# Performance work log

Hardware: AMD Instinct MI355X
Metric: run time of the kernel (lower is better)

The kernel has to match this reference:

```python
import jax, jax.numpy as jnp
import numpy as np

P = 2  # pooling_size

def setup_inputs() -> dict:
    key = jax.random.key(0)
    k1, k2, k3 = jax.random.split(key, 3)
    B, n, D = 16, 4096, 1024
    x = jax.random.normal(k1, (B, n, D), dtype=jnp.float32)
    W1 = jax.random.normal(k2, (D, D), dtype=jnp.float32) * (1.0 / np.sqrt(D))
    b1 = jnp.zeros((D,), dtype=jnp.float32)
    W2 = jax.random.normal(k3, (D, 1), dtype=jnp.float32) * (1.0 / np.sqrt(D))
    b2 = jnp.zeros((1,), dtype=jnp.float32)
    return {"x": x, "W1": W1, "b1": b1, "W2": W2, "b2": b2}

def reference(x, W1, b1, W2, b2):
    # x: [B, n, D] with n a perfect square; pool 2x2 windows via attention.
    B, n, D = x.shape
    s = int(n ** 0.5)
    g = s // P  # grid of regions per side
    # [B, g, P, g, P, D] -> [B, g, g, P, P, D] -> [B, R, P*P, D]
    # region order matches the original double loop (row-major over i, j).
    xg = (x.reshape(B, g, P, g, P, D)
            .transpose(0, 1, 3, 2, 4, 5)
            .reshape(B, g * g, P * P, D))
    # MLP scores (dropout is identity in eval mode)
    h = jax.nn.relu(jnp.einsum('brkd,de->brke', xg, W1) + b1)
    logits = jnp.einsum('brkd,d->brk', h, W2[:, 0]) + b2[0]
    alpha = jax.nn.softmax(logits, axis=-1)  # softmax over the P*P window
    # weighted sum over window -> [B, R, D]
    return jnp.einsum('brk,brkd->brd', alpha, xg)
```

## Files before the change

### kernel.cpp

```cpp
#include <hip/hip_runtime.h>
#include <hip/hip_bf16.h>

typedef float f32x4 __attribute__((ext_vector_type(4)));
typedef __bf16 bf16x8 __attribute__((ext_vector_type(8)));
typedef unsigned short ushort_t;
typedef ushort_t u16x8 __attribute__((ext_vector_type(8)));

#define GLDS16(gp, lp)                                                        \
  __builtin_amdgcn_global_load_lds(                                           \
      (__attribute__((address_space(1))) void*)(gp),                          \
      (__attribute__((address_space(3))) void*)(lp), 16, 0, 0)

__device__ __forceinline__ ushort_t f2bf(float f) {
  unsigned u = __float_as_uint(f);
  unsigned r = u + 0x7fffu + ((u >> 16) & 1u);
  return (ushort_t)(r >> 16);
}

__device__ __forceinline__ int swz(int row) {
  return (row & 3) ^ ((row >> 2) & 3);
}

__global__ __launch_bounds__(256) void prep_w1(const float* __restrict__ w1,
                                               ushort_t* __restrict__ w1t) {
  __shared__ ushort_t tile[64][80];
  const int k0 = blockIdx.x * 64;
  const int n0 = blockIdx.y * 64;
  const int tid = threadIdx.x;
#pragma unroll
  for (int it = 0; it < 16; ++it) {
    int idx = it * 256 + tid;
    int k = idx >> 6, n = idx & 63;
    tile[n][k] = f2bf(w1[(size_t)(k0 + k) * 1024 + n0 + n]);
  }
  __syncthreads();
#pragma unroll
  for (int it = 0; it < 2; ++it) {
    int idx = it * 256 + tid;
    int n = idx >> 3, kk = (idx & 7) * 8;
    bf16x8 v = *(const bf16x8*)&tile[n][kk];
    *(bf16x8*)&w1t[(size_t)(n0 + n) * 1024 + k0 + kk] = v;
  }
}

__global__ __launch_bounds__(256) void prep_x(const float* __restrict__ x,
                                              ushort_t* __restrict__ xbf) {
  size_t i = ((size_t)blockIdx.x * 256 + threadIdx.x) * 8;
  float4 a = *(const float4*)(x + i);
  float4 b = *(const float4*)(x + i + 4);
  u16x8 o;
  o[0] = f2bf(a.x); o[1] = f2bf(a.y); o[2] = f2bf(a.z); o[3] = f2bf(a.w);
  o[4] = f2bf(b.x); o[5] = f2bf(b.y); o[6] = f2bf(b.z); o[7] = f2bf(b.w);
  *(u16x8*)(xbf + i) = o;
}

#define FOLD_EPILOGUE(ACC, NH)                                                \
  {                                                                           \
    float bv[4], wv[4];                                                       \
    _Pragma("unroll") for (int ni = 0; ni < 4; ++ni) {                        \
      int col = nt * 256 + (NH)*128 + wn + ni * 16 + lc;                      \
      bv[ni] = b1[col];                                                       \
      wv[ni] = w2[col];                                                       \
    }                                                                         \
    _Pragma("unroll") for (int mi = 0; mi < 4; ++mi)                          \
        _Pragma("unroll") for (int r = 0; r < 4; ++r) {                       \
      float s = 0.f;                                                          \
      _Pragma("unroll") for (int ni = 0; ni < 4; ++ni) {                      \
        float h = ACC[mi][ni][r] + bv[ni];                                    \
        h = h > 0.f ? h : 0.f;                                                \
        s += h * wv[ni];                                                      \
      }                                                                       \
      racc[mi][r] += s;                                                       \
    }                                                                         \
  }

template <bool A_BF16>
__global__ __launch_bounds__(256, 2) void gemm_fused(
    const void* __restrict__ aglob, const ushort_t* __restrict__ w1t,
    const float* __restrict__ b1, const float* __restrict__ w2,
    const float* __restrict__ x, float* __restrict__ out) {
  __shared__ ushort_t As[2][128 * 32];
  __shared__ ushort_t Bs0[2][128 * 32];
  __shared__ ushort_t Bs1[2][128 * 32];
  __shared__ float lbuf[128];
  __shared__ float abuf[128];

  const int tid = threadIdx.x;
  const int wave = tid >> 6, lane = tid & 63;
  const int quad = lane >> 4, lc = lane & 15;
  const int m0 = blockIdx.x * 128;
  const int wm = (wave & 1) * 64, wn = (wave >> 1) * 64;

  const int g0 = tid, g1 = 256 + tid;
  const int r0 = g0 >> 2, c0 = (g0 & 3) ^ swz(g0 >> 2);
  const int r1 = g1 >> 2, c1 = (g1 & 3) ^ swz(g1 >> 2);
  const ushort_t* abf0 = nullptr; const ushort_t* abf1 = nullptr;
  const float* af0 = nullptr; const float* af1 = nullptr;
  if constexpr (A_BF16) {
    abf0 = (const ushort_t*)aglob + (size_t)(m0 + r0) * 1024 + c0 * 8;
    abf1 = (const ushort_t*)aglob + (size_t)(m0 + r1) * 1024 + c1 * 8;
  } else {
    af0 = (const float*)aglob + (size_t)(m0 + r0) * 1024 + c0 * 8;
    af1 = (const float*)aglob + (size_t)(m0 + r1) * 1024 + c1 * 8;
  }
  const ushort_t* b00 = w1t + (size_t)r0 * 1024 + c0 * 8;
  const ushort_t* b01 = w1t + (size_t)r1 * 1024 + c1 * 8;
  const ushort_t* b10 = w1t + (size_t)(128 + r0) * 1024 + c0 * 8;
  const ushort_t* b11 = w1t + (size_t)(128 + r1) * 1024 + c1 * 8;

  int aoff[4], boff[4];
#pragma unroll
  for (int mi = 0; mi < 4; ++mi) {
    int r = wm + mi * 16 + lc;
    aoff[mi] = r * 32 + (quad ^ swz(r)) * 8;
  }
#pragma unroll
  for (int ni = 0; ni < 4; ++ni) {
    int r = wn + ni * 16 + lc;
    boff[ni] = r * 32 + (quad ^ swz(r)) * 8;
  }

  auto stage = [&](int buf, int nt_, int kt_) {
    const size_t cb = (size_t)nt_ * (256 * 1024);
    const int k0 = kt_ * 32;
    GLDS16(b00 + cb + k0, &Bs0[buf][g0 * 8]);
    GLDS16(b01 + cb + k0, &Bs0[buf][g1 * 8]);
    GLDS16(b10 + cb + k0, &Bs1[buf][g0 * 8]);
    GLDS16(b11 + cb + k0, &Bs1[buf][g1 * 8]);
    if constexpr (A_BF16) {
      GLDS16(abf0 + k0, &As[buf][g0 * 8]);
      GLDS16(abf1 + k0, &As[buf][g1 * 8]);
    } else {
      const int k0f = kt_ * 32;
      float4 v0 = *(const float4*)(af0 + k0f);
      float4 v1 = *(const float4*)(af0 + k0f + 4);
      float4 v2 = *(const float4*)(af1 + k0f);
      float4 v3 = *(const float4*)(af1 + k0f + 4);
      u16x8 o0, o1;
      o0[0] = f2bf(v0.x); o0[1] = f2bf(v0.y); o0[2] = f2bf(v0.z); o0[3] = f2bf(v0.w);
      o0[4] = f2bf(v1.x); o0[5] = f2bf(v1.y); o0[6] = f2bf(v1.z); o0[7] = f2bf(v1.w);
      o1[0] = f2bf(v2.x); o1[1] = f2bf(v2.y); o1[2] = f2bf(v2.z); o1[3] = f2bf(v2.w);
      o1[4] = f2bf(v3.x); o1[5] = f2bf(v3.y); o1[6] = f2bf(v3.z); o1[7] = f2bf(v3.w);
      *(u16x8*)&As[buf][g0 * 8] = o0;
      *(u16x8*)&As[buf][g1 * 8] = o1;
    }
  };

  float racc[4][4] = {};

  stage(0, 0, 0);
  __syncthreads();

  for (int nt = 0; nt < 4; ++nt) {
    f32x4 acc0[4][4] = {};
    f32x4 acc1[4][4] = {};
#pragma unroll 2
    for (int kt = 0; kt < 32; ++kt) {
      const int cur = kt & 1;
      if (!(nt == 3 && kt == 31)) {
        int nk = kt + 1, nn = nt;
        if (nk == 32) { nk = 0; nn = nt + 1; }
        stage(cur ^ 1, nn, nk);
      }

      bf16x8 afr[4], bfr0[4], bfr1[4];
#pragma unroll
      for (int mi = 0; mi < 4; ++mi) afr[mi] = *(const bf16x8*)&As[cur][aoff[mi]];
#pragma unroll
      for (int ni = 0; ni < 4; ++ni) {
        bfr0[ni] = *(const bf16x8*)&Bs0[cur][boff[ni]];
        bfr1[ni] = *(const bf16x8*)&Bs1[cur][boff[ni]];
      }
#pragma unroll
      for (int mi = 0; mi < 4; ++mi)
#pragma unroll
        for (int ni = 0; ni < 4; ++ni) {
          acc0[mi][ni] = __builtin_amdgcn_mfma_f32_16x16x32_bf16(
              afr[mi], bfr0[ni], acc0[mi][ni], 0, 0, 0);
          acc1[mi][ni] = __builtin_amdgcn_mfma_f32_16x16x32_bf16(
              afr[mi], bfr1[ni], acc1[mi][ni], 0, 0, 0);
        }
      __syncthreads();
    }
    FOLD_EPILOGUE(acc0, 0)
    FOLD_EPILOGUE(acc1, 1)
  }

#pragma unroll
  for (int mi = 0; mi < 4; ++mi)
#pragma unroll
    for (int r = 0; r < 4; ++r)
#pragma unroll
      for (int off = 1; off < 16; off <<= 1)
        racc[mi][r] += __shfl_xor(racc[mi][r], off, 64);
  __syncthreads();
  if (tid < 128) lbuf[tid] = 0.f;
  __syncthreads();
  if (lc == 0) {
#pragma unroll
    for (int mi = 0; mi < 4; ++mi)
#pragma unroll
      for (int r = 0; r < 4; ++r)
        atomicAdd(&lbuf[wm + mi * 16 + quad * 4 + r], racc[mi][r]);
  }
  __syncthreads();

  if (tid < 32) {
    const int j = tid;
    float l0 = lbuf[2 * j], l1 = lbuf[2 * j + 1];
    float l2 = lbuf[64 + 2 * j], l3 = lbuf[65 + 2 * j];
    float mx = fmaxf(fmaxf(l0, l1), fmaxf(l2, l3));
    float e0 = __expf(l0 - mx), e1 = __expf(l1 - mx);
    float e2 = __expf(l2 - mx), e3 = __expf(l3 - mx);
    float inv = 1.0f / (e0 + e1 + e2 + e3);
    abuf[j * 4 + 0] = e0 * inv;
    abuf[j * 4 + 1] = e1 * inv;
    abuf[j * 4 + 2] = e2 * inv;
    abuf[j * 4 + 3] = e3 * inv;
  }
  __syncthreads();

  const int b = blockIdx.x >> 5, ii = blockIdx.x & 31;
  const float* xs = x + (size_t)m0 * 1024;
  float* orow = out + ((size_t)(b * 1024 + ii * 32)) * 1024;
  for (int j = 0; j < 32; ++j) {
    float a0 = abuf[j * 4 + 0], a1 = abuf[j * 4 + 1];
    float a2 = abuf[j * 4 + 2], a3 = abuf[j * 4 + 3];
    const float4* p0 = (const float4*)(xs + (size_t)(2 * j) * 1024);
    const float4* p1 = (const float4*)(xs + (size_t)(2 * j + 1) * 1024);
    const float4* p2 = (const float4*)(xs + (size_t)(64 + 2 * j) * 1024);
    const float4* p3 = (const float4*)(xs + (size_t)(65 + 2 * j) * 1024);
    float4 v0 = p0[tid], v1 = p1[tid], v2 = p2[tid], v3 = p3[tid];
    float4 o;
    o.x = a0 * v0.x + a1 * v1.x + a2 * v2.x + a3 * v3.x;
    o.y = a0 * v0.y + a1 * v1.y + a2 * v2.y + a3 * v3.y;
    o.z = a0 * v0.z + a1 * v1.z + a2 * v2.z + a3 * v3.z;
    o.w = a0 * v0.w + a1 * v1.w + a2 * v2.w + a3 * v3.w;
    ((float4*)(orow + (size_t)j * 1024))[tid] = o;
  }
}

extern "C" void kernel_launch(void* const* d_in, const int* in_sizes, int n_in,
                              void* d_out, int out_size, void* d_ws,
                              size_t ws_size, hipStream_t stream) {
  const float* x  = (const float*)d_in[0];
  const float* W1 = (const float*)d_in[1];
  const float* b1 = (const float*)d_in[2];
  const float* W2 = (const float*)d_in[3];
  float* out = (float*)d_out;

  const size_t XBF_BYTES = 134217728ull;
  const size_t W1T_BYTES = 2097152ull;

  if (ws_size >= XBF_BYTES + W1T_BYTES) {
    ushort_t* xbf = (ushort_t*)d_ws;
    ushort_t* w1t = (ushort_t*)((char*)d_ws + XBF_BYTES);
    prep_x<<<32768, 256, 0, stream>>>(x, xbf);
    prep_w1<<<dim3(16, 16), 256, 0, stream>>>(W1, w1t);
    gemm_fused<true><<<512, 256, 0, stream>>>(xbf, w1t, b1, W2, x, out);
  } else {
    ushort_t* w1t = (ushort_t*)d_ws;
    prep_w1<<<dim3(16, 16), 256, 0, stream>>>(W1, w1t);
    gemm_fused<false><<<512, 256, 0, stream>>>(x, w1t, b1, W2, x, out);
  }
}
```

Baseline: 583.2 us.

## Split fused GEMM block across eight waves with halved per-wave N tile

Doubles the block from 256 to 512 threads. Each wave now computes one 64x64 accumulator tile instead of two, and the two B sub-buffers are merged into one 256-row LDS tile. Global-to-LDS staging and the final weighted-sum loop are spread over the larger thread count. The aim is lower per-wave register pressure and more resident waves to hide memory and MFMA latency. In exchange, each A fragment is now read from LDS by twice as many waves, and the 512,4 launch bound may force spills if 128 VGPRs is not enough.

```diff
diff --git a/kernel.cpp b/kernel.cpp
--- a/kernel.cpp
+++ b/kernel.cpp
@@ -54,11 +54,11 @@
   *(u16x8*)(xbf + i) = o;
 }
 
-#define FOLD_EPILOGUE(ACC, NH)                                                \
+#define FOLD_EPILOGUE(ACC)                                                    \
   {                                                                           \
     float bv[4], wv[4];                                                       \
     _Pragma("unroll") for (int ni = 0; ni < 4; ++ni) {                        \
-      int col = nt * 256 + (NH)*128 + wn + ni * 16 + lc;                      \
+      int col = nt * 256 + wn + ni * 16 + lc;                                 \
       bv[ni] = b1[col];                                                       \
       wv[ni] = w2[col];                                                       \
     }                                                                         \
@@ -75,13 +75,12 @@
   }
 
 template <bool A_BF16>
-__global__ __launch_bounds__(256, 2) void gemm_fused(
+__global__ __launch_bounds__(512, 4) void gemm_fused(
     const void* __restrict__ aglob, const ushort_t* __restrict__ w1t,
     const float* __restrict__ b1, const float* __restrict__ w2,
     const float* __restrict__ x, float* __restrict__ out) {
   __shared__ ushort_t As[2][128 * 32];
-  __shared__ ushort_t Bs0[2][128 * 32];
-  __shared__ ushort_t Bs1[2][128 * 32];
+  __shared__ ushort_t Bs[2][256 * 32];
   __shared__ float lbuf[128];
   __shared__ float abuf[128];
 
@@ -91,22 +90,19 @@
   const int m0 = blockIdx.x * 128;
   const int wm = (wave & 1) * 64, wn = (wave >> 1) * 64;
 
-  const int g0 = tid, g1 = 256 + tid;
-  const int r0 = g0 >> 2, c0 = (g0 & 3) ^ swz(g0 >> 2);
-  const int r1 = g1 >> 2, c1 = (g1 & 3) ^ swz(g1 >> 2);
-  const ushort_t* abf0 = nullptr; const ushort_t* abf1 = nullptr;
-  const float* af0 = nullptr; const float* af1 = nullptr;
+  const int rA = tid >> 2, cA = (tid & 3) ^ swz(tid >> 2);
+  const int rB0 = tid >> 2, cB0 = (tid & 3) ^ swz(rB0);
+  const int rB1 = 128 + (tid >> 2), cB1 = (tid & 3) ^ swz(rB1);
+
+  const ushort_t* abf = nullptr;
+  const float* af = nullptr;
   if constexpr (A_BF16) {
-    abf0 = (const ushort_t*)aglob + (size_t)(m0 + r0) * 1024 + c0 * 8;
-    abf1 = (const ushort_t*)aglob + (size_t)(m0 + r1) * 1024 + c1 * 8;
+    abf = (const ushort_t*)aglob + (size_t)(m0 + rA) * 1024 + cA * 8;
   } else {
-    af0 = (const float*)aglob + (size_t)(m0 + r0) * 1024 + c0 * 8;
-    af1 = (const float*)aglob + (size_t)(m0 + r1) * 1024 + c1 * 8;
-  }
-  const ushort_t* b00 = w1t + (size_t)r0 * 1024 + c0 * 8;
-  const ushort_t* b01 = w1t + (size_t)r1 * 1024 + c1 * 8;
-  const ushort_t* b10 = w1t + (size_t)(128 + r0) * 1024 + c0 * 8;
-  const ushort_t* b11 = w1t + (size_t)(128 + r1) * 1024 + c1 * 8;
+    af = (const float*)aglob + (size_t)(m0 + rA) * 1024 + cA * 8;
+  }
+  const ushort_t* bp0 = w1t + (size_t)rB0 * 1024 + cB0 * 8;
+  const ushort_t* bp1 = w1t + (size_t)rB1 * 1024 + cB1 * 8;
 
   int aoff[4], boff[4];
 #pragma unroll
@@ -123,26 +119,17 @@
   auto stage = [&](int buf, int nt_, int kt_) {
     const size_t cb = (size_t)nt_ * (256 * 1024);
     const int k0 = kt_ * 32;
-    GLDS16(b00 + cb + k0, &Bs0[buf][g0 * 8]);
-    GLDS16(b01 + cb + k0, &Bs0[buf][g1 * 8]);
-    GLDS16(b10 + cb + k0, &Bs1[buf][g0 * 8]);
-    GLDS16(b11 + cb + k0, &Bs1[buf][g1 * 8]);
+    GLDS16(bp0 + cb + k0, &Bs[buf][tid * 8]);
+    GLDS16(bp1 + cb + k0, &Bs[buf][(512 + tid) * 8]);
     if constexpr (A_BF16) {
-      GLDS16(abf0 + k0, &As[buf][g0 * 8]);
-      GLDS16(abf1 + k0, &As[buf][g1 * 8]);
+      GLDS16(abf + k0, &As[buf][tid * 8]);
     } else {
-      const int k0f = kt_ * 32;
-      float4 v0 = *(const float4*)(af0 + k0f);
-      float4 v1 = *(const float4*)(af0 + k0f + 4);
-      float4 v2 = *(const float4*)(af1 + k0f);
-      float4 v3 = *(const float4*)(af1 + k0f + 4);
-      u16x8 o0, o1;
+      float4 v0 = *(const float4*)(af + k0);
+      float4 v1 = *(const float4*)(af + k0 + 4);
+      u16x8 o0;
       o0[0] = f2bf(v0.x); o0[1] = f2bf(v0.y); o0[2] = f2bf(v0.z); o0[3] = f2bf(v0.w);
       o0[4] = f2bf(v1.x); o0[5] = f2bf(v1.y); o0[6] = f2bf(v1.z); o0[7] = f2bf(v1.w);
-      o1[0] = f2bf(v2.x); o1[1] = f2bf(v2.y); o1[2] = f2bf(v2.z); o1[3] = f2bf(v2.w);
-      o1[4] = f2bf(v3.x); o1[5] = f2bf(v3.y); o1[6] = f2bf(v3.z); o1[7] = f2bf(v3.w);
-      *(u16x8*)&As[buf][g0 * 8] = o0;
-      *(u16x8*)&As[buf][g1 * 8] = o1;
+      *(u16x8*)&As[buf][tid * 8] = o0;
     }
   };
 
@@ -152,8 +139,7 @@
   __syncthreads();
 
   for (int nt = 0; nt < 4; ++nt) {
-    f32x4 acc0[4][4] = {};
-    f32x4 acc1[4][4] = {};
+    f32x4 acc[4][4] = {};
 #pragma unroll 2
     for (int kt = 0; kt < 32; ++kt) {
       const int cur = kt & 1;
@@ -163,27 +149,20 @@
         stage(cur ^ 1, nn, nk);
       }
 
-      bf16x8 afr[4], bfr0[4], bfr1[4];
+      bf16x8 afr[4], bfr[4];
 #pragma unroll
       for (int mi = 0; mi < 4; ++mi) afr[mi] = *(const bf16x8*)&As[cur][aoff[mi]];
 #pragma unroll
-      for (int ni = 0; ni < 4; ++ni) {
-        bfr0[ni] = *(const bf16x8*)&Bs0[cur][boff[ni]];
-        bfr1[ni] = *(const bf16x8*)&Bs1[cur][boff[ni]];
-      }
+      for (int ni = 0; ni < 4; ++ni) bfr[ni] = *(const bf16x8*)&Bs[cur][boff[ni]];
 #pragma unroll
       for (int mi = 0; mi < 4; ++mi)
 #pragma unroll
-        for (int ni = 0; ni < 4; ++ni) {
-          acc0[mi][ni] = __builtin_amdgcn_mfma_f32_16x16x32_bf16(
-              afr[mi], bfr0[ni], acc0[mi][ni], 0, 0, 0);
-          acc1[mi][ni] = __builtin_amdgcn_mfma_f32_16x16x32_bf16(
-              afr[mi], bfr1[ni], acc1[mi][ni], 0, 0, 0);
-        }
+        for (int ni = 0; ni < 4; ++ni)
+          acc[mi][ni] = __builtin_amdgcn_mfma_f32_16x16x32_bf16(
+              afr[mi], bfr[ni], acc[mi][ni], 0, 0, 0);
       __syncthreads();
     }
-    FOLD_EPILOGUE(acc0, 0)
-    FOLD_EPILOGUE(acc1, 1)
+    FOLD_EPILOGUE(acc)
   }
 
 #pragma unroll
@@ -221,22 +200,24 @@
   __syncthreads();
 
   const int b = blockIdx.x >> 5, ii = blockIdx.x & 31;
+  const int jj = tid >> 8, t = tid & 255;
   const float* xs = x + (size_t)m0 * 1024;
   float* orow = out + ((size_t)(b * 1024 + ii * 32)) * 1024;
-  for (int j = 0; j < 32; ++j) {
+  for (int j0 = 0; j0 < 32; j0 += 2) {
+    int j = j0 + jj;
     float a0 = abuf[j * 4 + 0], a1 = abuf[j * 4 + 1];
     float a2 = abuf[j * 4 + 2], a3 = abuf[j * 4 + 3];
     const float4* p0 = (const float4*)(xs + (size_t)(2 * j) * 1024);
     const float4* p1 = (const float4*)(xs + (size_t)(2 * j + 1) * 1024);
     const float4* p2 = (const float4*)(xs + (size_t)(64 + 2 * j) * 1024);
     const float4* p3 = (const float4*)(xs + (size_t)(65 + 2 * j) * 1024);
-    float4 v0 = p0[tid], v1 = p1[tid], v2 = p2[tid], v3 = p3[tid];
+    float4 v0 = p0[t], v1 = p1[t], v2 = p2[t], v3 = p3[t];
     float4 o;
     o.x = a0 * v0.x + a1 * v1.x + a2 * v2.x + a3 * v3.x;
     o.y = a0 * v0.y + a1 * v1.y + a2 * v2.y + a3 * v3.y;
     o.z = a0 * v0.z + a1 * v1.z + a2 * v2.z + a3 * v3.z;
     o.w = a0 * v0.w + a1 * v1.w + a2 * v2.w + a3 * v3.w;
-    ((float4*)(orow + (size_t)j * 1024))[tid] = o;
+    ((float4*)(orow + (size_t)j * 1024))[t] = o;
   }
 }
 
@@ -257,10 +238,10 @@
     ushort_t* w1t = (ushort_t*)((char*)d_ws + XBF_BYTES);
     prep_x<<<32768, 256, 0, stream>>>(x, xbf);
     prep_w1<<<dim3(16, 16), 256, 0, stream>>>(W1, w1t);
-    gemm_fused<true><<<512, 256, 0, stream>>>(xbf, w1t, b1, W2, x, out);
+    gemm_fused<true><<<512, 512, 0, stream>>>(xbf, w1t, b1, W2, x, out);
   } else {
     ushort_t* w1t = (ushort_t*)d_ws;
     prep_w1<<<dim3(16, 16), 256, 0, stream>>>(W1, w1t);
-    gemm_fused<false><<<512, 256, 0, stream>>>(x, w1t, b1, W2, x, out);
-  }
-}
+    gemm_fused<false><<<512, 512, 0, stream>>>(x, w1t, b1, W2, x, out);
+  }
+}
```

Result: no change. 581.2 us (-0.3%).
